# Optimization experiments

Measured on AMD Instinct MI355X. Metric: run time of the kernel, lower is better.

The kernel has to match this reference:

```python
import jax, jax.numpy as jnp
import numpy as np

B, T, D, H = 131072, 16, 2, 64  # batch, horizon, event dim, GRU hidden


def setup_inputs() -> dict:
    key = jax.random.key(0)
    ks = jax.random.split(key, 10)
    s = 1.0 / np.sqrt(H)
    u = lambda k, shape: jax.random.uniform(k, shape, jnp.float32, -s, s)
    return {
        "x": jax.random.normal(ks[0], (B, T, D), jnp.float32),   # base-dist samples
        "z": jax.random.normal(ks[1], (B, H), jnp.float32),      # context / GRU state
        # nn.GRUCell(input_size=D, hidden_size=H) params (torch layout)
        "W_ih": u(ks[2], (3 * H, D)),
        "W_hh": u(ks[3], (3 * H, H)),
        "b_ih": u(ks[4], (3 * H,)),
        "b_hh": u(ks[5], (3 * H,)),
        # locscale MLP: H -> 32 -> 4
        "W1": u(ks[6], (H, 32)),
        "b1": u(ks[7], (32,)),
        "W2": u(ks[8], (32, 4)),
        "b2": u(ks[9], (4,)),
    }


def reference(x, z, W_ih, W_hh, b_ih, b_hh, W1, b1, W2, b2):
    """AutoregressiveFlow._forward: base samples x -> data samples y, logabsdet."""
    Bb, Tt, Dd = x.shape

    def gru(inp, h):  # PyTorch GRUCell semantics
        gi = inp @ W_ih.T + b_ih          # [B, 3H]
        gh = h @ W_hh.T + b_hh            # [B, 3H]
        i_r, i_z, i_n = jnp.split(gi, 3, axis=-1)
        h_r, h_z, h_n = jnp.split(gh, 3, axis=-1)
        r = jax.nn.sigmoid(i_r + h_r)
        u = jax.nn.sigmoid(i_z + h_z)
        n = jnp.tanh(i_n + r * h_n)
        return (1.0 - u) * n + u * h

    def step(carry, x_t):
        h, y_tm1 = carry
        h = gru(y_tm1, h)
        hid = jax.nn.relu(h @ W1 + b1)            # [B, 32]
        ls = hid @ W2 + b2                        # [B, 4]
        dloc = ls[:, :2]
        scale = jax.nn.softplus(ls[:, 2:]) + 0.001
        y_t = y_tm1 + dloc + scale * x_t
        return (h, y_t), (y_t, scale)

    init = (z, jnp.zeros((Bb, Dd), x.dtype))
    _, (y, scales) = jax.lax.scan(step, init, jnp.swapaxes(x, 0, 1))
    y = jnp.swapaxes(y, 0, 1)          # [B, T, D]
    scales = jnp.swapaxes(scales, 0, 1)
    logabsdet = jnp.sum(jnp.log(jnp.abs(jnp.prod(scales, axis=-2))), axis=-1)  # [B]
    return y, logabsdet
```

## Files before the change

kernel.cpp:

```cpp
#include <hip/hip_runtime.h>

#define BSZ 131072
#define TT  16
#define RPB 64
#define BLK 256

#define LOG2E      1.4426950408889634f
#define NEG_LOG2E  (-1.4426950408889634f)
#define TWO_LOG2E  2.8853900817779268f

typedef __bf16 bf16x8 __attribute__((ext_vector_type(8)));
typedef float  f32x4  __attribute__((ext_vector_type(4)));

#define MFMA(a,b,c) __builtin_amdgcn_mfma_f32_16x16x32_bf16((a),(b),(c),0,0,0)

static __device__ __forceinline__ float rcp_f(float v){ float r; asm("v_rcp_f32 %0, %1" : "=v"(r) : "v"(v)); return r; }
static __device__ __forceinline__ float exp2_f(float v){ float r; asm("v_exp_f32 %0, %1" : "=v"(r) : "v"(v)); return r; }

__global__ __launch_bounds__(BLK, 3) void flow9(
    const float* __restrict__ x,
    const float* __restrict__ z,
    const float* __restrict__ W_ih,
    const float* __restrict__ W_hh,
    const float* __restrict__ b_ih,
    const float* __restrict__ b_hh,
    const float* __restrict__ W1,
    const float* __restrict__ b1,
    const float* __restrict__ W2,
    const float* __restrict__ b2,
    float* __restrict__ y_out,
    float* __restrict__ lad_out)
{
  __shared__ __align__(16) __bf16 whhtab[16*64*8];
  __shared__ __align__(16) __bf16 w1tab[4*64*8];
  __shared__ __align__(16) float4 gi_tab[192];
  __shared__ __align__(16) __bf16 hbuf[RPB*72];
  __shared__ __align__(16) __bf16 hidbuf[RPB*40];
  __shared__ __align__(16) float  ystate[RPB*2];

  const int tid  = threadIdx.x;
  const int lane = tid & 63, wave = tid >> 6;
  const int quad = lane >> 4, n16 = lane & 15;
  const int gb   = blockIdx.x * RPB;
  const f32x4 zero = {0.f,0.f,0.f,0.f};

  if (tid < 192) {
    const int j = tid;
    const float sc = (j < 128) ? NEG_LOG2E : TWO_LOG2E;
    const float w0 = W_ih[2*j]*sc, w1 = W_ih[2*j+1]*sc;
    const float bi = b_ih[j], bh = b_hh[j];
    gi_tab[j] = make_float4(w0, w1, ((j < 128) ? bi + bh : bi)*sc, 0.f);
  }
  #pragma unroll
  for (int i = 0; i < 4; ++i) {
    const int f = i*4 + wave;
    const int gate = 1 + (f >> 3), g = (f >> 1) & 3, kt = f & 1;
    const float sc = (gate == 1) ? NEG_LOG2E : TWO_LOG2E;
    const float* p = W_hh + (size_t)((gate*4 + g)*16 + n16)*64 + kt*32 + quad*8;
    bf16x8 v;
    #pragma unroll
    for (int j = 0; j < 8; ++j) v[j] = (__bf16)(p[j]*sc);
    *(bf16x8*)&whhtab[(f*64 + lane)*8] = v;
  }
  {
    const int f = wave, c2 = f >> 1, kt = f & 1;
    bf16x8 v;
    #pragma unroll
    for (int j = 0; j < 8; ++j)
      v[j] = (__bf16)W1[(size_t)(kt*32 + quad*8 + j)*32 + c2*16 + n16];
    *(bf16x8*)&w1tab[(f*64 + lane)*8] = v;
  }
  if (tid < 128) ystate[tid] = 0.f;
  #pragma unroll
  for (int r4 = 0; r4 < 4; ++r4) {
    const int row = (tid >> 4) + r4*16, col = (tid & 15)*4;
    const float4 zv = *(const float4*)&z[(size_t)(gb + row)*64 + col];
    hbuf[row*72 + col+0] = (__bf16)zv.x; hbuf[row*72 + col+1] = (__bf16)zv.y;
    hbuf[row*72 + col+2] = (__bf16)zv.z; hbuf[row*72 + col+3] = (__bf16)zv.w;
  }

  bf16x8 Whr[4][2];
  #pragma unroll
  for (int g = 0; g < 4; ++g)
    #pragma unroll
    for (int kt = 0; kt < 2; ++kt) {
      const float* p = W_hh + (size_t)(g*16 + n16)*64 + kt*32 + quad*8;
      bf16x8 v;
      #pragma unroll
      for (int j = 0; j < 8; ++j) v[j] = (__bf16)(p[j]*NEG_LOG2E);
      Whr[g][kt] = v;
    }
  bf16x8 W2f;
  #pragma unroll
  for (int j = 0; j < 8; ++j)
    W2f[j] = (n16 < 4) ? (__bf16)W2[(size_t)(quad*8 + j)*4 + n16] : (__bf16)0.f;

  f32x4 hst[4];
  #pragma unroll
  for (int g = 0; g < 4; ++g)
    #pragma unroll
    for (int i = 0; i < 4; ++i)
      hst[g][i] = z[(size_t)(gb + wave*16 + quad*4 + i)*64 + g*16 + n16];
  float bhn[4];
  #pragma unroll
  for (int g = 0; g < 4; ++g) bhn[g] = b_hh[128 + g*16 + n16]*TWO_LOG2E;
  const float b1v0 = b1[n16], b1v1 = b1[16 + n16];
  const float b2ln = (n16 < 4) ? b2[n16] : 0.f;

  __syncthreads();

  const int arow = wave*16 + n16;
  bf16x8 a0 = *(const bf16x8*)&hbuf[arow*72 + quad*8];
  bf16x8 a1 = *(const bf16x8*)&hbuf[arow*72 + 32 + quad*8];

  const int erow = wave*16 + (lane & 15);
  const int comp = (lane >> 4) & 1;
  const float* xp = x + (size_t)(gb + erow)*(TT*2) + comp;
  float*       yp = y_out + (size_t)(gb + erow)*(TT*2) + comp;
  float yc = 0.f, prodS = 1.0f;

  #pragma unroll 1
  for (int t = 0; t < TT; ++t) {
    const float xt = (lane < 32) ? xp[t*2] : 0.f;
    float ys0[4], ys1[4];
    #pragma unroll
    for (int i = 0; i < 4; ++i) {
      const float2 yv = *(const float2*)&ystate[(wave*16 + quad*4 + i)*2];
      ys0[i] = yv.x; ys1[i] = yv.y;
    }

    #pragma unroll
    for (int g = 0; g < 4; ++g) {
      const bf16x8 bz0 = *(const bf16x8*)&whhtab[((g*2    )*64 + lane)*8];
      const bf16x8 bz1 = *(const bf16x8*)&whhtab[((g*2 + 1)*64 + lane)*8];
      const bf16x8 bn0 = *(const bf16x8*)&whhtab[((8 + g*2    )*64 + lane)*8];
      const bf16x8 bn1 = *(const bf16x8*)&whhtab[((8 + g*2 + 1)*64 + lane)*8];
      f32x4 cr = MFMA(a0, Whr[g][0], zero); cr = MFMA(a1, Whr[g][1], cr);
      f32x4 cz = MFMA(a0, bz0, zero);       cz = MFMA(a1, bz1, cz);
      const f32x4 cninit = {bhn[g], bhn[g], bhn[g], bhn[g]};
      f32x4 cn = MFMA(a0, bn0, cninit);     cn = MFMA(a1, bn1, cn);
      const float4 Tr = gi_tab[      g*16 + n16];
      const float4 Tz = gi_tab[ 64 + g*16 + n16];
      const float4 Tn = gi_tab[128 + g*16 + n16];
      #pragma unroll
      for (int i = 0; i < 4; ++i) {
        const float sr  = fmaf(Tr.x, ys0[i], fmaf(Tr.y, ys1[i], Tr.z)) + cr[i];
        const float sz  = fminf(fmaf(Tz.x, ys0[i], fmaf(Tz.y, ys1[i], Tz.z)) + cz[i], 61.f);
        const float gin = fmaf(Tn.x, ys0[i], fmaf(Tn.y, ys1[i], Tn.z));
        const float r   = rcp_f(1.0f + exp2_f(sr));
        const float pre = fminf(fmaf(r, cn[i], gin), 61.f);
        const float Ez  = exp2_f(sz);
        const float En  = exp2_f(pre);
        const float S   = En + 1.0f;
        const float num = fmaf(S, hst[g][i] + Ez, Ez * -2.0f);
        const float den = fmaf(S, Ez, S);
        const float hv  = num * rcp_f(den);
        hst[g][i] = hv;
        hbuf[(wave*16 + quad*4 + i)*72 + g*16 + n16] = (__bf16)hv;
      }
    }

    a0 = *(const bf16x8*)&hbuf[arow*72 + quad*8];
    a1 = *(const bf16x8*)&hbuf[arow*72 + 32 + quad*8];

    #pragma unroll
    for (int c2 = 0; c2 < 2; ++c2) {
      const float bb = c2 ? b1v1 : b1v0;
      const f32x4 binit = {bb, bb, bb, bb};
      f32x4 hc = MFMA(a0, *(const bf16x8*)&w1tab[((c2*2  )*64 + lane)*8], binit);
      hc       = MFMA(a1, *(const bf16x8*)&w1tab[((c2*2+1)*64 + lane)*8], hc);
      #pragma unroll
      for (int i = 0; i < 4; ++i)
        hidbuf[(wave*16 + quad*4 + i)*40 + c2*16 + n16] = (__bf16)fmaxf(hc[i], 0.f);
    }

    {
      const bf16x8 ha = *(const bf16x8*)&hidbuf[arow*40 + quad*8];
      const f32x4 b2init = {b2ln, b2ln, b2ln, b2ln};
      const f32x4 ls = MFMA(ha, W2f, b2init);
      if (n16 < 4) {
        #pragma unroll
        for (int i = 0; i < 4; ++i)
          ((float*)&hidbuf[(wave*16 + quad*4 + i)*40 + 32])[n16] = ls[i];
      }
    }

    if (lane < 32) {
      const float* lsp = (const float*)&hidbuf[erow*40 + 32];
      const float lc = lsp[comp];
      const float l2 = lsp[2 + comp];
      const float s  = __logf(1.0f + __expf(l2)) + 0.001f;
      yc += lc + s * xt;
      prodS *= s;
      ystate[erow*2 + comp] = yc;
      yp[t*2] = yc;
    }
  }

  const float ll  = __logf(prodS);
  const float llo = __shfl(ll, lane ^ 16, 64);
  if (lane < 16) lad_out[gb + wave*16 + lane] = ll + llo;
}

extern "C" void kernel_launch(void* const* d_in, const int* in_sizes, int n_in,
                              void* d_out, int out_size, void* d_ws, size_t ws_size,
                              hipStream_t stream) {
  const float* x    = (const float*)d_in[0];
  const float* z    = (const float*)d_in[1];
  const float* W_ih = (const float*)d_in[2];
  const float* W_hh = (const float*)d_in[3];
  const float* b_ih = (const float*)d_in[4];
  const float* b_hh = (const float*)d_in[5];
  const float* W1   = (const float*)d_in[6];
  const float* b1   = (const float*)d_in[7];
  const float* W2   = (const float*)d_in[8];
  const float* b2   = (const float*)d_in[9];

  float* y_out   = (float*)d_out;
  float* lad_out = y_out + (size_t)BSZ * TT * 2;

  dim3 grid(BSZ / RPB), block(BLK);
  hipLaunchKernelGGL(flow9, grid, block, 0, stream,
                     x, z, W_ih, W_hh, b_ih, b_hh, W1, b1, W2, b2,
                     y_out, lad_out);
}
```

Baseline: 240.5 us.

## Process two 16-row tiles per wave to reuse weight fragments and add ILP

Doubles rows per block from 64 to 128 so each wave handles two independent 16-row tiles (A and B) through the GRU, MLP and output stages. The LDS-loaded weight fragments and gate tables are shared across both tiles, and the two independent MFMA/transcendental chains can interleave to hide latency. All 64 lanes now do the output update instead of half. The cost is roughly double the accumulator and state registers, which may hurt occupancy under the launch bound, and half as many blocks.

```diff
diff --git a/kernel.cpp b/kernel.cpp
--- a/kernel.cpp
+++ b/kernel.cpp
@@ -2,10 +2,9 @@
 
 #define BSZ 131072
 #define TT  16
-#define RPB 64
+#define RPB 128
 #define BLK 256
 
-#define LOG2E      1.4426950408889634f
 #define NEG_LOG2E  (-1.4426950408889634f)
 #define TWO_LOG2E  2.8853900817779268f
 
@@ -17,7 +16,21 @@
 static __device__ __forceinline__ float rcp_f(float v){ float r; asm("v_rcp_f32 %0, %1" : "=v"(r) : "v"(v)); return r; }
 static __device__ __forceinline__ float exp2_f(float v){ float r; asm("v_exp_f32 %0, %1" : "=v"(r) : "v"(v)); return r; }
 
-__global__ __launch_bounds__(BLK, 3) void flow9(
+#define GRU_ELEM(SR_IN, SZ_IN, GIN, CN_I, HREF, OUTROW)                        \
+  {                                                                            \
+    const float r_   = rcp_f(1.0f + exp2_f(SR_IN));                            \
+    const float pre_ = fminf(fmaf(r_, CN_I, GIN), 61.f);                       \
+    const float Ez_  = exp2_f(SZ_IN);                                          \
+    const float En_  = exp2_f(pre_);                                           \
+    const float S_   = En_ + 1.0f;                                             \
+    const float num_ = fmaf(S_, HREF + Ez_, Ez_ * -2.0f);                      \
+    const float den_ = fmaf(S_, Ez_, S_);                                      \
+    const float hv_  = num_ * rcp_f(den_);                                     \
+    HREF = hv_;                                                                \
+    hbuf[(OUTROW)*72 + g*16 + n16] = (__bf16)hv_;                              \
+  }
+
+__global__ __launch_bounds__(BLK, 3) void flow15(
     const float* __restrict__ x,
     const float* __restrict__ z,
     const float* __restrict__ W_ih,
@@ -70,9 +83,9 @@
       v[j] = (__bf16)W1[(size_t)(kt*32 + quad*8 + j)*32 + c2*16 + n16];
     *(bf16x8*)&w1tab[(f*64 + lane)*8] = v;
   }
-  if (tid < 128) ystate[tid] = 0.f;
-  #pragma unroll
-  for (int r4 = 0; r4 < 4; ++r4) {
+  ystate[tid] = 0.f;
+  #pragma unroll
+  for (int r4 = 0; r4 < 8; ++r4) {
     const int row = (tid >> 4) + r4*16, col = (tid & 15)*4;
     const float4 zv = *(const float4*)&z[(size_t)(gb + row)*64 + col];
     hbuf[row*72 + col+0] = (__bf16)zv.x; hbuf[row*72 + col+1] = (__bf16)zv.y;
@@ -95,12 +108,16 @@
   for (int j = 0; j < 8; ++j)
     W2f[j] = (n16 < 4) ? (__bf16)W2[(size_t)(quad*8 + j)*4 + n16] : (__bf16)0.f;
 
-  f32x4 hst[4];
+  const int trowA = wave*16 + quad*4;
+  const int trowB = 64 + trowA;
+  f32x4 hstA[4], hstB[4];
   #pragma unroll
   for (int g = 0; g < 4; ++g)
     #pragma unroll
-    for (int i = 0; i < 4; ++i)
-      hst[g][i] = z[(size_t)(gb + wave*16 + quad*4 + i)*64 + g*16 + n16];
+    for (int i = 0; i < 4; ++i) {
+      hstA[g][i] = z[(size_t)(gb + trowA + i)*64 + g*16 + n16];
+      hstB[g][i] = z[(size_t)(gb + trowB + i)*64 + g*16 + n16];
+    }
   float bhn[4];
   #pragma unroll
   for (int g = 0; g < 4; ++g) bhn[g] = b_hh[128 + g*16 + n16]*TWO_LOG2E;
@@ -109,24 +126,31 @@
 
   __syncthreads();
 
-  const int arow = wave*16 + n16;
-  bf16x8 a0 = *(const bf16x8*)&hbuf[arow*72 + quad*8];
-  bf16x8 a1 = *(const bf16x8*)&hbuf[arow*72 + 32 + quad*8];
-
-  const int erow = wave*16 + (lane & 15);
+  const int arowA = wave*16 + n16;
+  const int arowB = 64 + arowA;
+  bf16x8 a0A = *(const bf16x8*)&hbuf[arowA*72 + quad*8];
+  bf16x8 a1A = *(const bf16x8*)&hbuf[arowA*72 + 32 + quad*8];
+  bf16x8 a0B = *(const bf16x8*)&hbuf[arowB*72 + quad*8];
+  bf16x8 a1B = *(const bf16x8*)&hbuf[arowB*72 + 32 + quad*8];
+
+  const int half = lane >> 5;
+  const int erl  = lane & 15;
   const int comp = (lane >> 4) & 1;
+  const int erow = half*64 + wave*16 + erl;
   const float* xp = x + (size_t)(gb + erow)*(TT*2) + comp;
   float*       yp = y_out + (size_t)(gb + erow)*(TT*2) + comp;
   float yc = 0.f, prodS = 1.0f;
 
   #pragma unroll 1
   for (int t = 0; t < TT; ++t) {
-    const float xt = (lane < 32) ? xp[t*2] : 0.f;
-    float ys0[4], ys1[4];
+    const float xt = xp[t*2];
+    float ysA0[4], ysA1[4], ysB0[4], ysB1[4];
     #pragma unroll
     for (int i = 0; i < 4; ++i) {
-      const float2 yv = *(const float2*)&ystate[(wave*16 + quad*4 + i)*2];
-      ys0[i] = yv.x; ys1[i] = yv.y;
+      const float2 ya = *(const float2*)&ystate[(trowA + i)*2];
+      const float2 yb = *(const float2*)&ystate[(trowB + i)*2];
+      ysA0[i] = ya.x; ysA1[i] = ya.y;
+      ysB0[i] = yb.x; ysB1[i] = yb.y;
     }
 
     #pragma unroll
@@ -135,57 +159,67 @@
       const bf16x8 bz1 = *(const bf16x8*)&whhtab[((g*2 + 1)*64 + lane)*8];
       const bf16x8 bn0 = *(const bf16x8*)&whhtab[((8 + g*2    )*64 + lane)*8];
       const bf16x8 bn1 = *(const bf16x8*)&whhtab[((8 + g*2 + 1)*64 + lane)*8];
-      f32x4 cr = MFMA(a0, Whr[g][0], zero); cr = MFMA(a1, Whr[g][1], cr);
-      f32x4 cz = MFMA(a0, bz0, zero);       cz = MFMA(a1, bz1, cz);
-      const f32x4 cninit = {bhn[g], bhn[g], bhn[g], bhn[g]};
-      f32x4 cn = MFMA(a0, bn0, cninit);     cn = MFMA(a1, bn1, cn);
       const float4 Tr = gi_tab[      g*16 + n16];
       const float4 Tz = gi_tab[ 64 + g*16 + n16];
       const float4 Tn = gi_tab[128 + g*16 + n16];
+      const f32x4 cninit = {bhn[g], bhn[g], bhn[g], bhn[g]};
+
+      f32x4 crA = MFMA(a0A, Whr[g][0], zero); crA = MFMA(a1A, Whr[g][1], crA);
+      f32x4 crB = MFMA(a0B, Whr[g][0], zero); crB = MFMA(a1B, Whr[g][1], crB);
+      f32x4 czA = MFMA(a0A, bz0, zero);       czA = MFMA(a1A, bz1, czA);
+      f32x4 czB = MFMA(a0B, bz0, zero);       czB = MFMA(a1B, bz1, czB);
+      f32x4 cnA = MFMA(a0A, bn0, cninit);     cnA = MFMA(a1A, bn1, cnA);
+      f32x4 cnB = MFMA(a0B, bn0, cninit);     cnB = MFMA(a1B, bn1, cnB);
+
       #pragma unroll
       for (int i = 0; i < 4; ++i) {
-        const float sr  = fmaf(Tr.x, ys0[i], fmaf(Tr.y, ys1[i], Tr.z)) + cr[i];
-        const float sz  = fminf(fmaf(Tz.x, ys0[i], fmaf(Tz.y, ys1[i], Tz.z)) + cz[i], 61.f);
-        const float gin = fmaf(Tn.x, ys0[i], fmaf(Tn.y, ys1[i], Tn.z));
-        const float r   = rcp_f(1.0f + exp2_f(sr));
-        const float pre = fminf(fmaf(r, cn[i], gin), 61.f);
-        const float Ez  = exp2_f(sz);
-        const float En  = exp2_f(pre);
-        const float S   = En + 1.0f;
-        const float num = fmaf(S, hst[g][i] + Ez, Ez * -2.0f);
-        const float den = fmaf(S, Ez, S);
-        const float hv  = num * rcp_f(den);
-        hst[g][i] = hv;
-        hbuf[(wave*16 + quad*4 + i)*72 + g*16 + n16] = (__bf16)hv;
+        const float srA  = fmaf(Tr.x, ysA0[i], fmaf(Tr.y, ysA1[i], Tr.z)) + crA[i];
+        const float szA  = fminf(fmaf(Tz.x, ysA0[i], fmaf(Tz.y, ysA1[i], Tz.z)) + czA[i], 61.f);
+        const float ginA = fmaf(Tn.x, ysA0[i], fmaf(Tn.y, ysA1[i], Tn.z));
+        GRU_ELEM(srA, szA, ginA, cnA[i], hstA[g][i], trowA + i);
+        const float srB  = fmaf(Tr.x, ysB0[i], fmaf(Tr.y, ysB1[i], Tr.z)) + crB[i];
+        const float szB  = fminf(fmaf(Tz.x, ysB0[i], fmaf(Tz.y, ysB1[i], Tz.z)) + czB[i], 61.f);
+        const float ginB = fmaf(Tn.x, ysB0[i], fmaf(Tn.y, ysB1[i], Tn.z));
+        GRU_ELEM(srB, szB, ginB, cnB[i], hstB[g][i], trowB + i);
       }
     }
 
-    a0 = *(const bf16x8*)&hbuf[arow*72 + quad*8];
-    a1 = *(const bf16x8*)&hbuf[arow*72 + 32 + quad*8];
+    a0A = *(const bf16x8*)&hbuf[arowA*72 + quad*8];
+    a1A = *(const bf16x8*)&hbuf[arowA*72 + 32 + quad*8];
+    a0B = *(const bf16x8*)&hbuf[arowB*72 + quad*8];
+    a1B = *(const bf16x8*)&hbuf[arowB*72 + 32 + quad*8];
 
     #pragma unroll
     for (int c2 = 0; c2 < 2; ++c2) {
       const float bb = c2 ? b1v1 : b1v0;
       const f32x4 binit = {bb, bb, bb, bb};
-      f32x4 hc = MFMA(a0, *(const bf16x8*)&w1tab[((c2*2  )*64 + lane)*8], binit);
-      hc       = MFMA(a1, *(const bf16x8*)&w1tab[((c2*2+1)*64 + lane)*8], hc);
+      const bf16x8 wA = *(const bf16x8*)&w1tab[((c2*2  )*64 + lane)*8];
+      const bf16x8 wB = *(const bf16x8*)&w1tab[((c2*2+1)*64 + lane)*8];
+      f32x4 hcA = MFMA(a0A, wA, binit); hcA = MFMA(a1A, wB, hcA);
+      f32x4 hcB = MFMA(a0B, wA, binit); hcB = MFMA(a1B, wB, hcB);
       #pragma unroll
-      for (int i = 0; i < 4; ++i)
-        hidbuf[(wave*16 + quad*4 + i)*40 + c2*16 + n16] = (__bf16)fmaxf(hc[i], 0.f);
+      for (int i = 0; i < 4; ++i) {
+        hidbuf[(trowA + i)*40 + c2*16 + n16] = (__bf16)fmaxf(hcA[i], 0.f);
+        hidbuf[(trowB + i)*40 + c2*16 + n16] = (__bf16)fmaxf(hcB[i], 0.f);
+      }
     }
 
     {
-      const bf16x8 ha = *(const bf16x8*)&hidbuf[arow*40 + quad*8];
+      const bf16x8 haA = *(const bf16x8*)&hidbuf[arowA*40 + quad*8];
+      const bf16x8 haB = *(const bf16x8*)&hidbuf[arowB*40 + quad*8];
       const f32x4 b2init = {b2ln, b2ln, b2ln, b2ln};
-      const f32x4 ls = MFMA(ha, W2f, b2init);
+      const f32x4 lsA = MFMA(haA, W2f, b2init);
+      const f32x4 lsB = MFMA(haB, W2f, b2init);
       if (n16 < 4) {
         #pragma unroll
-        for (int i = 0; i < 4; ++i)
-          ((float*)&hidbuf[(wave*16 + quad*4 + i)*40 + 32])[n16] = ls[i];
+        for (int i = 0; i < 4; ++i) {
+          ((float*)&hidbuf[(trowA + i)*40 + 32])[n16] = lsA[i];
+          ((float*)&hidbuf[(trowB + i)*40 + 32])[n16] = lsB[i];
+        }
       }
     }
 
-    if (lane < 32) {
+    {
       const float* lsp = (const float*)&hidbuf[erow*40 + 32];
       const float lc = lsp[comp];
       const float l2 = lsp[2 + comp];
@@ -199,7 +233,8 @@
 
   const float ll  = __logf(prodS);
   const float llo = __shfl(ll, lane ^ 16, 64);
-  if (lane < 16) lad_out[gb + wave*16 + lane] = ll + llo;
+  if ((lane & 16) == 0)
+    lad_out[gb + half*64 + wave*16 + (lane & 15)] = ll + llo;
 }
 
 extern "C" void kernel_launch(void* const* d_in, const int* in_sizes, int n_in,
@@ -220,7 +255,7 @@
   float* lad_out = y_out + (size_t)BSZ * TT * 2;
 
   dim3 grid(BSZ / RPB), block(BLK);
-  hipLaunchKernelGGL(flow9, grid, block, 0, stream,
+  hipLaunchKernelGGL(flow15, grid, block, 0, stream,
                      x, z, W_ih, W_hh, b_ih, b_hh, W1, b1, W2, b2,
                      y_out, lad_out);
 }
```

New measurement: 375.3 us. 1.56x slower.
